# Kernel tuning notes

Measured on AMD Instinct MI355X. Metric: run time of the kernel, lower is better.

## Reference

```python
import jax, jax.numpy as jnp
import numpy as np
import math

B, T, C = 2, 512, 1024
E, TOPK = 8, 2
NH, HS = 8, 128  # att_hidden = NH*HS = 1024
AH = NH * HS


def setup_inputs() -> dict:
    key = jax.random.key(0)
    ks = jax.random.split(key, 8)
    s = 0.02
    return {
        "x": jax.random.normal(ks[0], (B, T, C), dtype=jnp.float32),
        "Wg": jax.random.normal(ks[1], (C, E), dtype=jnp.float32) * s,
        "W_in": jax.random.normal(ks[2], (E, C, AH), dtype=jnp.float32) * s,
        "W_out": jax.random.normal(ks[3], (E, AH, C), dtype=jnp.float32) * s,
        "Wk": jax.random.normal(ks[4], (C, AH), dtype=jnp.float32) * s,
        "bk": jnp.zeros((AH,), dtype=jnp.float32),
        "Wv": jax.random.normal(ks[5], (C, AH), dtype=jnp.float32) * s,
        "bv": jnp.zeros((AH,), dtype=jnp.float32),
    }


def stickbreaking(logits, mask, cum_weight):
    # logits: [B, i, j, k, h]; mask/cum_weight: [i, j] (tril / strict tril)
    log_z = jax.nn.log_sigmoid(logits)
    m = mask[None, :, :, None, None]
    log_beta = jnp.where(m == 0, 0.0, log_z - logits)  # log(1-sigmoid)
    # cumulative sum of log_beta over earlier positions: [b,i,j,n,h] x [j,k] -> [b,i,k,n,h]
    re_cum_log_beta = jnp.einsum('bijnh,jk->biknh', log_beta, cum_weight)
    return jnp.where(m == 0, 0.0, jnp.exp(log_z + re_cum_log_beta))


def reference(x, Wg, W_in, W_out, Wk, bk, Wv, bv):
    Bx, Tx, Cx = x.shape
    # --- MoE q_proj.map: top-k expert routing ---
    gate_logits = jnp.einsum('btc,ce->bte', x, Wg)
    top_vals, top_idx = jax.lax.top_k(gate_logits, TOPK)        # [B,T,K]
    gates = jax.nn.softmax(top_vals, axis=-1)                    # [B,T,K]
    all_q = jnp.einsum('btc,ech->bteh', x, W_in)                 # [B,T,E,AH]
    q = jnp.take_along_axis(all_q, top_idx[..., None], axis=2)   # [B,T,K,AH]
    # aux load-balancing loss (switch-style)
    probs = jax.nn.softmax(gate_logits, axis=-1)                 # [B,T,E]
    disp = jax.nn.one_hot(top_idx, E, dtype=x.dtype)             # [B,T,K,E]
    frac = disp.sum(axis=2).reshape(-1, E).mean(axis=0)
    aux_loss = E * jnp.sum(probs.reshape(-1, E).mean(axis=0) * frac)

    k = x @ Wk + bk
    v = x @ Wv + bv

    q = q.reshape(Bx, Tx, TOPK, NH, HS)
    k = k.reshape(Bx, Tx, NH, HS)
    v = v.reshape(Bx, Tx, NH, HS)

    tril = jnp.tril(jnp.ones((Tx, Tx), dtype=x.dtype))
    mask = tril                                   # history_length=0 -> ctx==T
    cum_weight = jnp.tril(tril, -1)

    att = jnp.einsum('bikhd,bjhd->bijkh', q, k) * (1.0 / math.sqrt(HS))
    att = stickbreaking(att, mask, cum_weight)    # [B,T,T,K,NH]

    y = jnp.einsum('bijkh,bjhd->bikhd', att, v)   # [B,T,K,NH,HS]
    y = y.reshape(Bx, Tx, TOPK, AH)

    # --- MoE q_proj.reduce: per-expert output proj, gate-weighted combine ---
    yw = y * gates[..., None]                     # [B,T,K,AH]
    comb = jnp.einsum('btkh,btke->bteh', yw, disp)  # [B,T,E,AH]
    out = jnp.einsum('bteh,ehc->btc', comb, W_out)  # [B,T,C]
    return out, aux_loss
```

## Files before the change

### kernel.cpp

```cpp
#include <hip/hip_runtime.h>
#include <cmath>

#define B_    2
#define T_    512
#define C_    1024
#define E_    8
#define NTOK  1024
#define NPAIR 2048
#define AH_   1024
#define NH_   8
#define HS_   128

typedef unsigned short u16;
typedef __attribute__((ext_vector_type(8))) short bf16x8;
typedef __attribute__((ext_vector_type(4))) float f32x4;

__device__ __forceinline__ u16 f2bf(float f) {
    union { float f; unsigned u; } v; v.f = f;
    unsigned r = v.u + 0x7fff + ((v.u >> 16) & 1);
    return (u16)(r >> 16);
}

typedef const __attribute__((address_space(1))) unsigned int ga_u32;
typedef __attribute__((address_space(3))) unsigned int ls_u32;
__device__ __forceinline__ void gld_lds16(const u16* g, u16* l) {
    __builtin_amdgcn_global_load_lds((ga_u32*)g, (ls_u32*)l, 16, 0, 0);
}

__device__ __forceinline__ void atomic_fadd(float* p, float v) {
    __hip_atomic_fetch_add(p, v, __ATOMIC_RELAXED, __HIP_MEMORY_SCOPE_AGENT);
}

__global__ __launch_bounds__(64) void gate_kernel(
    const float* __restrict__ x, const float* __restrict__ Wg,
    u16* __restrict__ xb, float* __restrict__ gates,
    float* __restrict__ probs, int* __restrict__ eass,
    float* __restrict__ out)
{
    int token = blockIdx.x;
    int lane  = threadIdx.x;
    {
        float4 z4 = {0.f, 0.f, 0.f, 0.f};
        float4* orow = (float4*)(out + (size_t)token * C_);
#pragma unroll
        for (int i = 0; i < 4; i++) orow[lane + i * 64] = z4;
    }
    const float* xr = x + (size_t)token * C_;
    u16* xbr = xb + (size_t)token * C_;
    float acc[E_];
#pragma unroll
    for (int e = 0; e < E_; e++) acc[e] = 0.f;
    for (int c = lane; c < C_; c += 64) {
        float xv = xr[c];
        xbr[c] = f2bf(xv);
        const float* wr = Wg + c * E_;
#pragma unroll
        for (int e = 0; e < E_; e++) acc[e] += xv * wr[e];
    }
#pragma unroll
    for (int e = 0; e < E_; e++) {
        float v = acc[e];
        v += __shfl_xor(v, 32); v += __shfl_xor(v, 16); v += __shfl_xor(v, 8);
        v += __shfl_xor(v, 4);  v += __shfl_xor(v, 2);  v += __shfl_xor(v, 1);
        acc[e] = v;
    }
    if (lane == 0) {
        int i0 = 0; float v0 = acc[0];
        for (int e = 1; e < E_; e++) if (acc[e] > v0) { v0 = acc[e]; i0 = e; }
        int i1 = -1; float v1 = -3.4e38f;
        for (int e = 0; e < E_; e++) if (e != i0 && acc[e] > v1) { v1 = acc[e]; i1 = e; }
        float e1  = __expf(v1 - v0);
        float inv = 1.f / (1.f + e1);
        gates[token * 2 + 0] = inv;
        gates[token * 2 + 1] = e1 * inv;
        float s = 0.f; float pe[E_];
        for (int e = 0; e < E_; e++) { pe[e] = __expf(acc[e] - v0); s += pe[e]; }
        float sinv = 1.f / s;
        for (int e = 0; e < E_; e++) probs[token * E_ + e] = pe[e] * sinv;
        eass[token * 2 + 0] = i0;
        eass[token * 2 + 1] = i1;
    }
}

__global__ __launch_bounds__(256) void route_kernel(
    const float* __restrict__ probs, const int* __restrict__ eass,
    const float* __restrict__ bk, const float* __restrict__ bv,
    int* __restrict__ bucket_cnt, int* __restrict__ buckets,
    float* __restrict__ bkv, float* __restrict__ aux_out)
{
    __shared__ float red[256][17];
    __shared__ int lcnt[E_];
    int tid = threadIdx.x;
    for (int i = tid; i < 1024; i += 256) {
        bkv[i] = bk[i];
        bkv[i + 1024] = bv[i];
    }
    float ps[E_], fc[E_];
#pragma unroll
    for (int e = 0; e < E_; e++) { ps[e] = 0.f; fc[e] = 0.f; }
    for (int k = 0; k < 4; k++) {
        int row = tid + k * 256;
#pragma unroll
        for (int e = 0; e < E_; e++) ps[e] += probs[row * E_ + e];
    }
    for (int k = 0; k < 8; k++) {
        int i = tid + k * 256;
        int ea = eass[i];
#pragma unroll
        for (int e = 0; e < E_; e++) fc[e] += (ea == e) ? 1.f : 0.f;
    }
#pragma unroll
    for (int e = 0; e < E_; e++) { red[tid][e] = ps[e]; red[tid][8 + e] = fc[e]; }
    if (tid < E_) lcnt[tid] = 0;
    __syncthreads();
    for (int s = 128; s > 0; s >>= 1) {
        if (tid < s)
#pragma unroll
            for (int j = 0; j < 16; j++) red[tid][j] += red[tid + s][j];
        __syncthreads();
    }
    if (tid == 0) {
        float s = 0.f;
        for (int e = 0; e < E_; e++)
            s += (red[0][e] * (1.f / 1024.f)) * (red[0][8 + e] * (1.f / 1024.f));
        aux_out[0] = (float)E_ * s;
    }
    for (int k = 0; k < 8; k++) {
        int i = tid + k * 256;
        int ea = eass[i];
        int pos = atomicAdd(&lcnt[ea], 1);
        buckets[ea * NPAIR + pos] = i;
    }
    __syncthreads();
    if (tid < E_) bucket_cnt[tid] = lcnt[tid];
}

__global__ __launch_bounds__(256) void pack_all(
    const float* __restrict__ Win, const float* __restrict__ Wout,
    const float* __restrict__ Wk, const float* __restrict__ Wv,
    u16* __restrict__ wp, u16* __restrict__ woutp, u16* __restrict__ wkvp)
{
    __shared__ float t[64][65];
    int z = blockIdx.z;
    const float* src; u16* dst;
    if (z < 8)       { src = Win  + ((size_t)z << 20);       dst = wp    + ((size_t)z << 20); }
    else if (z < 16) { src = Wout + ((size_t)(z - 8) << 20); dst = woutp + ((size_t)(z - 8) << 20); }
    else if (z == 16){ src = Wk;                             dst = wkvp; }
    else             { src = Wv;                             dst = wkvp + ((size_t)1 << 20); }
    int k0 = blockIdx.y * 64, n0 = blockIdx.x * 64;
    int tid = threadIdx.x;
#pragma unroll
    for (int p = 0; p < 4; p++) {
        int e4 = tid + 256 * p;
        int r = e4 >> 4, c4 = e4 & 15;
        float4 v = *(const float4*)&src[(size_t)(k0 + r) * 1024 + n0 + c4 * 4];
        t[r][c4 * 4 + 0] = v.x; t[r][c4 * 4 + 1] = v.y;
        t[r][c4 * 4 + 2] = v.z; t[r][c4 * 4 + 3] = v.w;
    }
    __syncthreads();
    int c = tid & 63, ks_rel = (tid >> 6) & 1, ph = tid >> 7;
    int n_glob = n0 + c, nt = n_glob >> 7, n_loc = n_glob & 127;
    int ks = (k0 >> 5) + ks_rel;
    u16* ob = dst + (((size_t)(nt * 32 + ks)) << 12) + n_loc * 32;
#pragma unroll
    for (int pp = 0; pp < 2; pp++) {
        int p = ph * 2 + pp;
        int g = (p - ((n_loc >> 1) & 3)) & 3;
        int kb = ks_rel * 32 + g * 8;
        ushort4 o1, o2;
        o1.x = f2bf(t[kb + 0][c]); o1.y = f2bf(t[kb + 1][c]);
        o1.z = f2bf(t[kb + 2][c]); o1.w = f2bf(t[kb + 3][c]);
        o2.x = f2bf(t[kb + 4][c]); o2.y = f2bf(t[kb + 5][c]);
        o2.z = f2bf(t[kb + 6][c]); o2.w = f2bf(t[kb + 7][c]);
        *(ushort4*)&ob[p * 8]     = o1;
        *(ushort4*)&ob[p * 8 + 4] = o2;
    }
}

__device__ __forceinline__ void mfma_lds_loop(
    const u16* __restrict__ Aptr,
    const u16* __restrict__ Bsrc,
    u16* __restrict__ ldsB,
    int tid, f32x4 acc[8])
{
    int w = tid >> 6, lane = tid & 63, lm = lane & 15, g = lane >> 4;
    int swz = (g + ((lm >> 1) & 3)) & 3;
    const u16* gstage = Bsrc + w * 512 + lane * 8;
    u16* lstage = ldsB + w * 512;
    const u16* bbase = ldsB + lm * 32 + swz * 8;

#pragma unroll
    for (int c = 0; c < 4; c++)
        gld_lds16(gstage + c * 2048, lstage + c * 2048);

    bf16x8 a0 = *(const bf16x8*)(Aptr);
    bf16x8 a1 = *(const bf16x8*)(Aptr + 32);
    __syncthreads();

#pragma unroll
    for (int kk = 0; kk < 16; kk++) {
        int cur = kk & 1;
        if (kk < 15) {
            const u16* gs = gstage + (size_t)(kk + 1) * 8192;
            u16* ls = lstage + ((kk + 1) & 1) * 8192;
#pragma unroll
            for (int c = 0; c < 4; c++)
                gld_lds16(gs + c * 2048, ls + c * 2048);
        }
        bf16x8 na0, na1;
        if (kk < 15) {
            na0 = *(const bf16x8*)(Aptr + (size_t)(2 * kk + 2) * 32);
            na1 = *(const bf16x8*)(Aptr + (size_t)(2 * kk + 3) * 32);
        }
        const u16* bb = bbase + cur * 8192;
#pragma unroll
        for (int j = 0; j < 8; j++) {
            bf16x8 b0 = *(const bf16x8*)(bb + j * 512);
            acc[j] = __builtin_amdgcn_mfma_f32_16x16x32_bf16(a0, b0, acc[j], 0, 0, 0);
        }
#pragma unroll
        for (int j = 0; j < 8; j++) {
            bf16x8 b1 = *(const bf16x8*)(bb + 4096 + j * 512);
            acc[j] = __builtin_amdgcn_mfma_f32_16x16x32_bf16(a1, b1, acc[j], 0, 0, 0);
        }
        a0 = na0; a1 = na1;
        __syncthreads();
    }
}

__global__ __launch_bounds__(256) void gemm_fused(
    const u16* __restrict__ xb, const u16* __restrict__ Wkv_p,
    const float* __restrict__ bkv, const u16* __restrict__ Win_p,
    const int* __restrict__ bucket_cnt, const int* __restrict__ buckets,
    u16* __restrict__ Kb, u16* __restrict__ Vb, u16* __restrict__ Qb)
{
    __shared__ __align__(16) u16 ldsB[2 * 8192];
    int bx = blockIdx.x;
    int tid = threadIdx.x;
    int w = tid >> 6, lane = tid & 63, lm = lane & 15, g = lane >> 4;
    bool isKV = bx < 256;
    int e = 0, mt, nt, cnt;
    const u16* Wp;
    if (isKV) {
        mt = bx & 15; nt = bx >> 4; cnt = NTOK; Wp = Wkv_p;
    } else {
        int b2 = bx - 256;
        mt = b2 >> 6; e = (b2 & 63) >> 3; nt = b2 & 7;
        cnt = bucket_cnt[e];
        Wp = Win_p + ((size_t)e << 20);
    }
    int m0 = mt * 64;
    if (m0 >= cnt) return;
    int strip = m0 + w * 16;

    int arow, drow[4];
    if (isKV) {
        arow = strip + lm;
#pragma unroll
        for (int r = 0; r < 4; r++) drow[r] = strip + g * 4 + r;
    } else {
        int ai = strip + lm;
        arow = buckets[e * NPAIR + (ai < cnt ? ai : cnt - 1)] >> 1;
#pragma unroll
        for (int r = 0; r < 4; r++) {
            int di = strip + g * 4 + r;
            drow[r] = (di < cnt) ? buckets[e * NPAIR + di] : -1;
        }
    }
    const u16* Aptr = xb + (size_t)arow * 1024 + g * 8;
    const u16* Bsrc = Wp + (((size_t)(nt * 32)) << 12);

    f32x4 acc[8];
#pragma unroll
    for (int j = 0; j < 8; j++) acc[j] = 0;

    mfma_lds_loop(Aptr, Bsrc, ldsB, tid, acc);

#pragma unroll
    for (int reg = 0; reg < 4; reg++) {
        int di = strip + g * 4 + reg;
        if (isKV || di < cnt) {
            int orow = drow[reg];
            if (!isKV && orow < 0) continue;
#pragma unroll
            for (int j = 0; j < 8; j++) {
                int col = nt * 128 + j * 16 + lm;
                float v = acc[j][reg];
                if (isKV) {
                    v += bkv[col];
                    int tb = orow >> 9, tj = orow & 511;
                    int cc = col & 1023;
                    int hh = cc >> 7, dd = cc & 127;
                    u16* dst = (col < 1024) ? Kb : Vb;
                    dst[(((size_t)(tb * 8 + hh) * 512 + tj) << 7) + dd] = f2bf(v);
                } else {
                    int pb = orow >> 10, pi = (orow >> 1) & 511, ps = orow & 1;
                    int hh = col >> 7, dd = col & 127;
                    Qb[((((size_t)(pb * 16 + ps * 8 + hh)) * 512 + pi) << 7) + dd] = f2bf(v);
                }
            }
        }
    }
}

__global__ __launch_bounds__(256) void gemm_wout(
    const u16* __restrict__ yb, const u16* __restrict__ Wout_p,
    const int* __restrict__ bucket_cnt, const int* __restrict__ buckets,
    float* __restrict__ Out)
{
    __shared__ __align__(16) u16 ldsB[2 * 8192];
    int bx = blockIdx.x;
    int tid = threadIdx.x;
    int w = tid >> 6, lane = tid & 63, lm = lane & 15, g = lane >> 4;
    int mt = bx >> 6, e = (bx & 63) >> 3, nt = bx & 7;
    int cnt = bucket_cnt[e];
    int m0 = mt * 64;
    if (m0 >= cnt) return;
    int strip = m0 + w * 16;

    int ai = strip + lm;
    int arow = buckets[e * NPAIR + (ai < cnt ? ai : cnt - 1)];
    int drow[4];
#pragma unroll
    for (int r = 0; r < 4; r++) {
        int di = strip + g * 4 + r;
        drow[r] = (di < cnt) ? buckets[e * NPAIR + di] : -1;
    }
    const u16* Aptr = yb + (size_t)arow * 1024 + g * 8;
    const u16* Bsrc = Wout_p + ((size_t)e << 20) + (((size_t)(nt * 32)) << 12);

    f32x4 acc[8];
#pragma unroll
    for (int j = 0; j < 8; j++) acc[j] = 0;

    mfma_lds_loop(Aptr, Bsrc, ldsB, tid, acc);

#pragma unroll
    for (int reg = 0; reg < 4; reg++) {
        int orow = drow[reg];
        if (orow >= 0) {
            float* od = Out + (size_t)(orow >> 1) * 1024;
#pragma unroll
            for (int j = 0; j < 8; j++) {
                int col = nt * 128 + j * 16 + lm;
                atomic_fadd(&od[col], acc[j][reg]);
            }
        }
    }
}

__global__ __launch_bounds__(256) void vtrans(
    const u16* __restrict__ Vb, u16* __restrict__ Vtb)
{
    __shared__ u16 t[64][72];
    int bh = blockIdx.x;
    int d0 = blockIdx.y * 64;
    int j0 = blockIdx.z * 64;
    int tid = threadIdx.x;
#pragma unroll
    for (int p = 0; p < 2; p++) {
        int c = tid + 256 * p;
        int jr = c >> 3, c8 = c & 7;
        *(bf16x8*)&t[jr][c8 * 8] =
            *(const bf16x8*)&Vb[((size_t)bh * 512 + j0 + jr) * 128 + d0 + c8 * 8];
    }
    __syncthreads();
#pragma unroll
    for (int p = 0; p < 2; p++) {
        int c = tid + 256 * p;
        int dr = c >> 3, j8 = c & 7;
        bf16x8 o;
#pragma unroll
        for (int k = 0; k < 8; k++) o[k] = (short)t[j8 * 8 + k][dr];
        *(bf16x8*)&Vtb[((size_t)bh * 128 + d0 + dr) * 512 + j0 + j8 * 8] = o;
    }
}

__global__ __launch_bounds__(256) void attn_kernel(
    const u16* __restrict__ Qb, const u16* __restrict__ Kb,
    const u16* __restrict__ Vtb, const float* __restrict__ gates,
    u16* __restrict__ yb)
{
    __shared__ __align__(16) u16 Qs[32 * 136];
    __shared__ __align__(16) u16 Ks[2][32 * 136];
    __shared__ __align__(16) u16 Vts[2][128 * 40];
    __shared__ __align__(16) float sw[32 * 36];
    __shared__ __align__(16) u16 wt[32 * 40];

    int combo = blockIdx.x;
    int b = combo >> 4, slot = (combo >> 3) & 1, h = combo & 7;
    int bh = b * 8 + h;
    const u16* Qbase = Qb  + ((size_t)combo << 16);
    const u16* Kbase = Kb  + ((size_t)bh << 16);
    const u16* Vbase = Vtb + ((size_t)bh << 16);

    int tid = threadIdx.x;
    int w = tid >> 6, lane = tid & 63, lm = lane & 15, g = lane >> 4;
    int mh = w >> 1, nh = w & 1, dsel = w & 1;
    int srow = tid >> 3, st = tid & 7;
    int rowlane = lane & 56;
    const float SCALE2 = 0.127517433f;

    int by = blockIdx.y;
    int it = (by < 8) ? (15 - by) : (by - 8);
    int i0 = it * 32;

    int kr0 = tid >> 4, kc = (tid & 15) * 8;
    int vr0 = tid >> 2, vc = (tid & 3) * 8;
    bf16x8 kreg[2], vreg[2];

#define LDKV(j0_)                                                                  \
    {                                                                              \
        _Pragma("unroll")                                                          \
        for (int p = 0; p < 2; p++) {                                              \
            kreg[p] = *(const bf16x8*)&Kbase[(size_t)((j0_) + kr0 + 16 * p) * 128 + kc]; \
            vreg[p] = *(const bf16x8*)&Vbase[(size_t)(vr0 + 64 * p) * 512 + (j0_) + vc]; \
        }                                                                          \
    }
#define STKV(buf_)                                                                 \
    {                                                                              \
        _Pragma("unroll")                                                          \
        for (int p = 0; p < 2; p++) {                                              \
            *(bf16x8*)&Ks[buf_][(kr0 + 16 * p) * 136 + kc] = kreg[p];              \
            *(bf16x8*)&Vts[buf_][(vr0 + 64 * p) * 40 + vc] = vreg[p];              \
        }                                                                          \
    }

#pragma unroll
    for (int p = 0; p < 2; p++) {
        int c = tid + 256 * p;
        int r = c >> 4, c8 = c & 15;
        *(bf16x8*)&Qs[r * 136 + c8 * 8] =
            *(const bf16x8*)&Qbase[(size_t)(i0 + r) * 128 + c8 * 8];
    }
    LDKV(i0);
    STKV(0);
    __syncthreads();

    f32x4 pacc[4];
#pragma unroll
    for (int q = 0; q < 4; q++) pacc[q] = 0;
    float running = 0.f;
    int pbuf = 0;

    for (int jt = it; jt >= 0; jt--) {
        int j0 = jt * 32;
        f32x4 sacc = 0;
#pragma unroll
        for (int ks = 0; ks < 4; ks++) {
            bf16x8 aq = *(const bf16x8*)&Qs[(mh * 16 + lm) * 136 + ks * 32 + g * 8];
            bf16x8 bk = *(const bf16x8*)&Ks[pbuf][(nh * 16 + lm) * 136 + ks * 32 + g * 8];
            sacc = __builtin_amdgcn_mfma_f32_16x16x32_bf16(aq, bk, sacc, 0, 0, 0);
        }
#pragma unroll
        for (int reg = 0; reg < 4; reg++)
            sw[(mh * 16 + g * 4 + reg) * 36 + nh * 16 + lm] = sacc[reg] * SCALE2;
        if (jt > 0) LDKV(j0 - 32);
        __syncthreads();
        {
            float4 sv = *(const float4*)&sw[srow * 36 + st * 4];
            float sarr[4] = {sv.x, sv.y, sv.z, sv.w};
            int ig = i0 + srow;
            float lsig[4], lb[4];
#pragma unroll
            for (int c2 = 0; c2 < 4; c2++) {
                int jg = j0 + st * 4 + c2;
                float sc = sarr[c2];
                float a  = fabsf(sc);
                float tl = __builtin_amdgcn_logf(1.f + __builtin_amdgcn_exp2f(-a));
                lsig[c2] = (sc >= 0.f) ? -tl : sc - tl;
                lb[c2]   = (jg <= ig) ? -(tl + fmaxf(sc, 0.f)) : 0.f;
            }
            float suf[4];
            suf[3] = 0.f;
            suf[2] = lb[3];
            suf[1] = lb[2] + lb[3];
            suf[0] = lb[1] + suf[1];
            float total = lb[0] + suf[0];
            float incl = total;
            float y1 = __shfl_down(incl, 1, 64); if (st < 7) incl += y1;
            float y2 = __shfl_down(incl, 2, 64); if (st < 6) incl += y2;
            float y4 = __shfl_down(incl, 4, 64); if (st < 4) incl += y4;
            float basev = (incl - total) + running;
            ushort4 wo;
            float wv;
            int jgc = j0 + st * 4;
            wv = (jgc + 0 <= ig) ? __builtin_amdgcn_exp2f(lsig[0] + suf[0] + basev) : 0.f; wo.x = f2bf(wv);
            wv = (jgc + 1 <= ig) ? __builtin_amdgcn_exp2f(lsig[1] + suf[1] + basev) : 0.f; wo.y = f2bf(wv);
            wv = (jgc + 2 <= ig) ? __builtin_amdgcn_exp2f(lsig[2] + suf[2] + basev) : 0.f; wo.z = f2bf(wv);
            wv = (jgc + 3 <= ig) ? __builtin_amdgcn_exp2f(lsig[3] + suf[3] + basev) : 0.f; wo.w = f2bf(wv);
            running += __shfl(incl, rowlane, 64);
            *(ushort4*)&wt[srow * 40 + st * 4] = wo;
        }
        if (jt > 0) STKV(pbuf ^ 1);
        __syncthreads();
        bf16x8 aw = *(const bf16x8*)&wt[(mh * 16 + lm) * 40 + g * 8];
#pragma unroll
        for (int q = 0; q < 4; q++) {
            int dt = q * 2 + dsel;
            bf16x8 bv8 = *(const bf16x8*)&Vts[pbuf][(dt * 16 + lm) * 40 + g * 8];
            pacc[q] = __builtin_amdgcn_mfma_f32_16x16x32_bf16(aw, bv8, pacc[q], 0, 0, 0);
        }
        pbuf ^= 1;
    }
#pragma unroll
    for (int reg = 0; reg < 4; reg++) {
        int i = i0 + mh * 16 + g * 4 + reg;
        size_t pair = ((size_t)(b * 512 + i)) * 2 + slot;
        float gt = gates[pair];
#pragma unroll
        for (int q = 0; q < 4; q++) {
            int d = (q * 2 + dsel) * 16 + lm;
            yb[pair * 1024 + h * 128 + d] = f2bf(pacc[q][reg] * gt);
        }
    }
#undef LDKV
#undef STKV
}

extern "C" void kernel_launch(void* const* d_in, const int* in_sizes, int n_in,
                              void* d_out, int out_size, void* d_ws, size_t ws_size,
                              hipStream_t stream)
{
    const float* x     = (const float*)d_in[0];
    const float* Wg    = (const float*)d_in[1];
    const float* W_in  = (const float*)d_in[2];
    const float* W_out = (const float*)d_in[3];
    const float* Wk    = (const float*)d_in[4];
    const float* bk    = (const float*)d_in[5];
    const float* Wv    = (const float*)d_in[6];
    const float* bv    = (const float*)d_in[7];

    char* ws = (char*)d_ws;
    int*   bucket_cnt = (int*)ws;
    size_t off = 256;
    float* gates = (float*)(ws + off); off += (size_t)NPAIR * 4;
    int* buckets = (int*)(ws + off);   off += (size_t)E_ * NPAIR * 4;
    float* bkv   = (float*)(ws + off); off += 2048 * 4;
    float* probs = (float*)(ws + off); off += (size_t)NTOK * E_ * 4;
    int*   eass  = (int*)(ws + off);   off += (size_t)NPAIR * 4;
    off = (off + 255) & ~(size_t)255;
    u16* xb     = (u16*)(ws + off); off += (size_t)NTOK * C_ * 2;
    u16* Wkv_p  = (u16*)(ws + off); off += (size_t)2048 * 1024 * 2;
    u16* wp     = (u16*)(ws + off); off += (size_t)E_ * 1024 * 1024 * 2;
    u16* wout_p = (u16*)(ws + off); off += (size_t)E_ * 1024 * 1024 * 2;
    u16* yb     = (u16*)(ws + off); off += (size_t)NPAIR * AH_ * 2;
    u16* Qbuf   = (u16*)(ws + off); off += (size_t)32 * 512 * 128 * 2;
    u16* Kbuf   = (u16*)(ws + off); off += (size_t)16 * 512 * 128 * 2;
    u16* Vbuf   = (u16*)(ws + off); off += (size_t)16 * 512 * 128 * 2;
    u16* Vtbuf  = (u16*)(ws + off); off += (size_t)16 * 128 * 512 * 2;

    gate_kernel<<<NTOK, 64, 0, stream>>>(x, Wg, xb, gates, probs, eass,
                                         (float*)d_out);
    route_kernel<<<1, 256, 0, stream>>>(probs, eass, bk, bv, bucket_cnt,
                                        buckets, bkv,
                                        (float*)d_out + (out_size - 1));
    pack_all<<<dim3(16, 16, 18), 256, 0, stream>>>(W_in, W_out, Wk, Wv,
                                                   wp, wout_p, Wkv_p);

    gemm_fused<<<256 + 2048, 256, 0, stream>>>(xb, Wkv_p, bkv, wp, bucket_cnt,
                                               buckets, Kbuf, Vbuf, Qbuf);
    vtrans<<<dim3(16, 2, 8), 256, 0, stream>>>(Vbuf, Vtbuf);

    attn_kernel<<<dim3(32, 16), 256, 0, stream>>>(Qbuf, Kbuf, Vtbuf, gates, yb);

    gemm_wout<<<2048, 256, 0, stream>>>(yb, wout_p, bucket_cnt, buckets,
                                        (float*)d_out);
}
```

Before: 206.6 us.

## Merge gate into weight-pack kernel and fuse V transpose into GEMM epilogue

The gating/x-to-bf16 kernel and the bias copy are folded into the weight packing kernel as extra blocks on a flattened 1D grid, so one launch replaces two. The V transpose kernel is removed: KV GEMM tiles for V columns are staged through LDS and written directly in transposed layout, avoiding a round trip through an intermediate V buffer. This reduces launch count and global traffic, but reuses the GEMM's LDS buffer after the MFMA loop and adds a branchy epilogue.

Result: faster. 198.5 us (-3.9%).

```diff
diff --git a/kernel.cpp b/kernel.cpp
--- a/kernel.cpp
+++ b/kernel.cpp
@@ -31,124 +31,82 @@
     __hip_atomic_fetch_add(p, v, __ATOMIC_RELAXED, __HIP_MEMORY_SCOPE_AGENT);
 }
 
-__global__ __launch_bounds__(64) void gate_kernel(
+__global__ __launch_bounds__(256) void pack_gate(
+    const float* __restrict__ Win, const float* __restrict__ Wout,
+    const float* __restrict__ Wk, const float* __restrict__ Wv,
+    u16* __restrict__ wp, u16* __restrict__ woutp, u16* __restrict__ wkvp,
     const float* __restrict__ x, const float* __restrict__ Wg,
     u16* __restrict__ xb, float* __restrict__ gates,
     float* __restrict__ probs, int* __restrict__ eass,
-    float* __restrict__ out)
-{
-    int token = blockIdx.x;
-    int lane  = threadIdx.x;
-    {
-        float4 z4 = {0.f, 0.f, 0.f, 0.f};
-        float4* orow = (float4*)(out + (size_t)token * C_);
-#pragma unroll
-        for (int i = 0; i < 4; i++) orow[lane + i * 64] = z4;
-    }
-    const float* xr = x + (size_t)token * C_;
-    u16* xbr = xb + (size_t)token * C_;
-    float acc[E_];
-#pragma unroll
-    for (int e = 0; e < E_; e++) acc[e] = 0.f;
-    for (int c = lane; c < C_; c += 64) {
-        float xv = xr[c];
-        xbr[c] = f2bf(xv);
-        const float* wr = Wg + c * E_;
-#pragma unroll
-        for (int e = 0; e < E_; e++) acc[e] += xv * wr[e];
-    }
-#pragma unroll
-    for (int e = 0; e < E_; e++) {
-        float v = acc[e];
-        v += __shfl_xor(v, 32); v += __shfl_xor(v, 16); v += __shfl_xor(v, 8);
-        v += __shfl_xor(v, 4);  v += __shfl_xor(v, 2);  v += __shfl_xor(v, 1);
-        acc[e] = v;
-    }
-    if (lane == 0) {
-        int i0 = 0; float v0 = acc[0];
-        for (int e = 1; e < E_; e++) if (acc[e] > v0) { v0 = acc[e]; i0 = e; }
-        int i1 = -1; float v1 = -3.4e38f;
-        for (int e = 0; e < E_; e++) if (e != i0 && acc[e] > v1) { v1 = acc[e]; i1 = e; }
-        float e1  = __expf(v1 - v0);
-        float inv = 1.f / (1.f + e1);
-        gates[token * 2 + 0] = inv;
-        gates[token * 2 + 1] = e1 * inv;
-        float s = 0.f; float pe[E_];
-        for (int e = 0; e < E_; e++) { pe[e] = __expf(acc[e] - v0); s += pe[e]; }
-        float sinv = 1.f / s;
-        for (int e = 0; e < E_; e++) probs[token * E_ + e] = pe[e] * sinv;
-        eass[token * 2 + 0] = i0;
-        eass[token * 2 + 1] = i1;
-    }
-}
-
-__global__ __launch_bounds__(256) void route_kernel(
-    const float* __restrict__ probs, const int* __restrict__ eass,
+    float* __restrict__ out,
     const float* __restrict__ bk, const float* __restrict__ bv,
-    int* __restrict__ bucket_cnt, int* __restrict__ buckets,
-    float* __restrict__ bkv, float* __restrict__ aux_out)
-{
-    __shared__ float red[256][17];
-    __shared__ int lcnt[E_];
+    float* __restrict__ bkv)
+{
+    __shared__ float t[64][65];
+    int bx = blockIdx.x;
     int tid = threadIdx.x;
-    for (int i = tid; i < 1024; i += 256) {
-        bkv[i] = bk[i];
-        bkv[i + 1024] = bv[i];
-    }
-    float ps[E_], fc[E_];
-#pragma unroll
-    for (int e = 0; e < E_; e++) { ps[e] = 0.f; fc[e] = 0.f; }
-    for (int k = 0; k < 4; k++) {
-        int row = tid + k * 256;
-#pragma unroll
-        for (int e = 0; e < E_; e++) ps[e] += probs[row * E_ + e];
-    }
-    for (int k = 0; k < 8; k++) {
-        int i = tid + k * 256;
-        int ea = eass[i];
-#pragma unroll
-        for (int e = 0; e < E_; e++) fc[e] += (ea == e) ? 1.f : 0.f;
-    }
-#pragma unroll
-    for (int e = 0; e < E_; e++) { red[tid][e] = ps[e]; red[tid][8 + e] = fc[e]; }
-    if (tid < E_) lcnt[tid] = 0;
-    __syncthreads();
-    for (int s = 128; s > 0; s >>= 1) {
-        if (tid < s)
-#pragma unroll
-            for (int j = 0; j < 16; j++) red[tid][j] += red[tid + s][j];
-        __syncthreads();
-    }
-    if (tid == 0) {
-        float s = 0.f;
-        for (int e = 0; e < E_; e++)
-            s += (red[0][e] * (1.f / 1024.f)) * (red[0][8 + e] * (1.f / 1024.f));
-        aux_out[0] = (float)E_ * s;
-    }
-    for (int k = 0; k < 8; k++) {
-        int i = tid + k * 256;
-        int ea = eass[i];
-        int pos = atomicAdd(&lcnt[ea], 1);
-        buckets[ea * NPAIR + pos] = i;
-    }
-    __syncthreads();
-    if (tid < E_) bucket_cnt[tid] = lcnt[tid];
-}
-
-__global__ __launch_bounds__(256) void pack_all(
-    const float* __restrict__ Win, const float* __restrict__ Wout,
-    const float* __restrict__ Wk, const float* __restrict__ Wv,
-    u16* __restrict__ wp, u16* __restrict__ woutp, u16* __restrict__ wkvp)
-{
-    __shared__ float t[64][65];
-    int z = blockIdx.z;
+
+    if (bx >= 4608) {
+        if (bx == 4864) {
+            for (int i = tid; i < 1024; i += 256) {
+                bkv[i] = bk[i];
+                bkv[i + 1024] = bv[i];
+            }
+            return;
+        }
+        int w = tid >> 6, lane = tid & 63;
+        int token = (bx - 4608) * 4 + w;
+        {
+            float4 z4 = {0.f, 0.f, 0.f, 0.f};
+            float4* orow = (float4*)(out + (size_t)token * C_);
+#pragma unroll
+            for (int i = 0; i < 4; i++) orow[lane + i * 64] = z4;
+        }
+        const float* xr = x + (size_t)token * C_;
+        u16* xbr = xb + (size_t)token * C_;
+        float acc[E_];
+#pragma unroll
+        for (int e = 0; e < E_; e++) acc[e] = 0.f;
+        for (int c = lane; c < C_; c += 64) {
+            float xv = xr[c];
+            xbr[c] = f2bf(xv);
+            const float* wr = Wg + c * E_;
+#pragma unroll
+            for (int e = 0; e < E_; e++) acc[e] += xv * wr[e];
+        }
+#pragma unroll
+        for (int e = 0; e < E_; e++) {
+            float v = acc[e];
+            v += __shfl_xor(v, 32); v += __shfl_xor(v, 16); v += __shfl_xor(v, 8);
+            v += __shfl_xor(v, 4);  v += __shfl_xor(v, 2);  v += __shfl_xor(v, 1);
+            acc[e] = v;
+        }
+        if (lane == 0) {
+            int i0 = 0; float v0 = acc[0];
+            for (int e = 1; e < E_; e++) if (acc[e] > v0) { v0 = acc[e]; i0 = e; }
+            int i1 = -1; float v1 = -3.4e38f;
+            for (int e = 0; e < E_; e++) if (e != i0 && acc[e] > v1) { v1 = acc[e]; i1 = e; }
+            float e1  = __expf(v1 - v0);
+            float inv = 1.f / (1.f + e1);
+            gates[token * 2 + 0] = inv;
+            gates[token * 2 + 1] = e1 * inv;
+            float s = 0.f; float pe[E_];
+            for (int e = 0; e < E_; e++) { pe[e] = __expf(acc[e] - v0); s += pe[e]; }
+            float sinv = 1.f / s;
+            for (int e = 0; e < E_; e++) probs[token * E_ + e] = pe[e] * sinv;
+            eass[token * 2 + 0] = i0;
+            eass[token * 2 + 1] = i1;
+        }
+        return;
+    }
+
+    int z = bx >> 8, yy = (bx >> 4) & 15, xx = bx & 15;
     const float* src; u16* dst;
-    if (z < 8)       { src = Win  + ((size_t)z << 20);       dst = wp    + ((size_t)z << 20); }
-    else if (z < 16) { src = Wout + ((size_t)(z - 8) << 20); dst = woutp + ((size_t)(z - 8) << 20); }
-    else if (z == 16){ src = Wk;                             dst = wkvp; }
-    else             { src = Wv;                             dst = wkvp + ((size_t)1 << 20); }
-    int k0 = blockIdx.y * 64, n0 = blockIdx.x * 64;
-    int tid = threadIdx.x;
+    if (z < 8)        { src = Win  + ((size_t)z << 20);       dst = wp    + ((size_t)z << 20); }
+    else if (z < 16)  { src = Wout + ((size_t)(z - 8) << 20); dst = woutp + ((size_t)(z - 8) << 20); }
+    else if (z == 16) { src = Wk;                             dst = wkvp; }
+    else              { src = Wv;                             dst = wkvp + ((size_t)1 << 20); }
+    int k0 = yy * 64, n0 = xx * 64;
 #pragma unroll
     for (int p = 0; p < 4; p++) {
         int e4 = tid + 256 * p;
@@ -177,6 +135,54 @@
     }
 }
 
+__global__ __launch_bounds__(256) void route_kernel(
+    const float* __restrict__ probs, const int* __restrict__ eass,
+    int* __restrict__ bucket_cnt, int* __restrict__ buckets,
+    float* __restrict__ aux_out)
+{
+    __shared__ float red[256][17];
+    __shared__ int lcnt[E_];
+    int tid = threadIdx.x;
+    float ps[E_], fc[E_];
+#pragma unroll
+    for (int e = 0; e < E_; e++) { ps[e] = 0.f; fc[e] = 0.f; }
+    for (int k = 0; k < 4; k++) {
+        int row = tid + k * 256;
+#pragma unroll
+        for (int e = 0; e < E_; e++) ps[e] += probs[row * E_ + e];
+    }
+    for (int k = 0; k < 8; k++) {
+        int i = tid + k * 256;
+        int ea = eass[i];
+#pragma unroll
+        for (int e = 0; e < E_; e++) fc[e] += (ea == e) ? 1.f : 0.f;
+    }
+#pragma unroll
+    for (int e = 0; e < E_; e++) { red[tid][e] = ps[e]; red[tid][8 + e] = fc[e]; }
+    if (tid < E_) lcnt[tid] = 0;
+    __syncthreads();
+    for (int s = 128; s > 0; s >>= 1) {
+        if (tid < s)
+#pragma unroll
+            for (int j = 0; j < 16; j++) red[tid][j] += red[tid + s][j];
+        __syncthreads();
+    }
+    if (tid == 0) {
+        float s = 0.f;
+        for (int e = 0; e < E_; e++)
+            s += (red[0][e] * (1.f / 1024.f)) * (red[0][8 + e] * (1.f / 1024.f));
+        aux_out[0] = (float)E_ * s;
+    }
+    for (int k = 0; k < 8; k++) {
+        int i = tid + k * 256;
+        int ea = eass[i];
+        int pos = atomicAdd(&lcnt[ea], 1);
+        buckets[ea * NPAIR + pos] = i;
+    }
+    __syncthreads();
+    if (tid < E_) bucket_cnt[tid] = lcnt[tid];
+}
+
 __device__ __forceinline__ void mfma_lds_loop(
     const u16* __restrict__ Aptr,
     const u16* __restrict__ Bsrc,
@@ -232,7 +238,7 @@
     const u16* __restrict__ xb, const u16* __restrict__ Wkv_p,
     const float* __restrict__ bkv, const u16* __restrict__ Win_p,
     const int* __restrict__ bucket_cnt, const int* __restrict__ buckets,
-    u16* __restrict__ Kb, u16* __restrict__ Vb, u16* __restrict__ Qb)
+    u16* __restrict__ Kb, u16* __restrict__ Vtb, u16* __restrict__ Qb)
 {
     __shared__ __align__(16) u16 ldsB[2 * 8192];
     int bx = blockIdx.x;
@@ -276,6 +282,33 @@
 
     mfma_lds_loop(Aptr, Bsrc, ldsB, tid, acc);
 
+    if (isKV && nt >= 8) {
+        u16* tt = ldsB;
+#pragma unroll
+        for (int reg = 0; reg < 4; reg++) {
+            int r_loc = w * 16 + g * 4 + reg;
+#pragma unroll
+            for (int j = 0; j < 8; j++) {
+                int col = nt * 128 + j * 16 + lm;
+                tt[r_loc * 136 + j * 16 + lm] = f2bf(acc[j][reg] + bkv[col]);
+            }
+        }
+        __syncthreads();
+        int hh = nt - 8;
+        int tb = m0 >> 9, tj0 = m0 & 511;
+        int bh = tb * 8 + hh;
+#pragma unroll
+        for (int p = 0; p < 4; p++) {
+            int cc = tid + 256 * p;
+            int dr = cc >> 3, j8 = cc & 7;
+            bf16x8 o;
+#pragma unroll
+            for (int k = 0; k < 8; k++) o[k] = (short)tt[(j8 * 8 + k) * 136 + dr];
+            *(bf16x8*)&Vtb[((size_t)bh * 128 + dr) * 512 + tj0 + j8 * 8] = o;
+        }
+        return;
+    }
+
 #pragma unroll
     for (int reg = 0; reg < 4; reg++) {
         int di = strip + g * 4 + reg;
@@ -289,10 +322,8 @@
                 if (isKV) {
                     v += bkv[col];
                     int tb = orow >> 9, tj = orow & 511;
-                    int cc = col & 1023;
-                    int hh = cc >> 7, dd = cc & 127;
-                    u16* dst = (col < 1024) ? Kb : Vb;
-                    dst[(((size_t)(tb * 8 + hh) * 512 + tj) << 7) + dd] = f2bf(v);
+                    int hh = col >> 7, dd = col & 127;
+                    Kb[(((size_t)(tb * 8 + hh) * 512 + tj) << 7) + dd] = f2bf(v);
                 } else {
                     int pb = orow >> 10, pi = (orow >> 1) & 511, ps = orow & 1;
                     int hh = col >> 7, dd = col & 127;
@@ -346,33 +377,6 @@
                 atomic_fadd(&od[col], acc[j][reg]);
             }
         }
-    }
-}
-
-__global__ __launch_bounds__(256) void vtrans(
-    const u16* __restrict__ Vb, u16* __restrict__ Vtb)
-{
-    __shared__ u16 t[64][72];
-    int bh = blockIdx.x;
-    int d0 = blockIdx.y * 64;
-    int j0 = blockIdx.z * 64;
-    int tid = threadIdx.x;
-#pragma unroll
-    for (int p = 0; p < 2; p++) {
-        int c = tid + 256 * p;
-        int jr = c >> 3, c8 = c & 7;
-        *(bf16x8*)&t[jr][c8 * 8] =
-            *(const bf16x8*)&Vb[((size_t)bh * 512 + j0 + jr) * 128 + d0 + c8 * 8];
-    }
-    __syncthreads();
-#pragma unroll
-    for (int p = 0; p < 2; p++) {
-        int c = tid + 256 * p;
-        int dr = c >> 3, j8 = c & 7;
-        bf16x8 o;
-#pragma unroll
-        for (int k = 0; k < 8; k++) o[k] = (short)t[j8 * 8 + k][dr];
-        *(bf16x8*)&Vtb[((size_t)bh * 128 + d0 + dr) * 512 + j0 + j8 * 8] = o;
     }
 }
 
@@ -547,20 +551,16 @@
     u16* yb     = (u16*)(ws + off); off += (size_t)NPAIR * AH_ * 2;
     u16* Qbuf   = (u16*)(ws + off); off += (size_t)32 * 512 * 128 * 2;
     u16* Kbuf   = (u16*)(ws + off); off += (size_t)16 * 512 * 128 * 2;
-    u16* Vbuf   = (u16*)(ws + off); off += (size_t)16 * 512 * 128 * 2;
     u16* Vtbuf  = (u16*)(ws + off); off += (size_t)16 * 128 * 512 * 2;
 
-    gate_kernel<<<NTOK, 64, 0, stream>>>(x, Wg, xb, gates, probs, eass,
-                                         (float*)d_out);
-    route_kernel<<<1, 256, 0, stream>>>(probs, eass, bk, bv, bucket_cnt,
-                                        buckets, bkv,
+    pack_gate<<<4865, 256, 0, stream>>>(W_in, W_out, Wk, Wv, wp, wout_p, Wkv_p,
+                                        x, Wg, xb, gates, probs, eass,
+                                        (float*)d_out, bk, bv, bkv);
+    route_kernel<<<1, 256, 0, stream>>>(probs, eass, bucket_cnt, buckets,
                                         (float*)d_out + (out_size - 1));
-    pack_all<<<dim3(16, 16, 18), 256, 0, stream>>>(W_in, W_out, Wk, Wv,
-                                                   wp, wout_p, Wkv_p);
 
     gemm_fused<<<256 + 2048, 256, 0, stream>>>(xb, Wkv_p, bkv, wp, bucket_cnt,
-                                               buckets, Kbuf, Vbuf, Qbuf);
-    vtrans<<<dim3(16, 2, 8), 256, 0, stream>>>(Vbuf, Vtbuf);
+                                               buckets, Kbuf, Vtbuf, Qbuf);
 
     attn_kernel<<<dim3(32, 16), 256, 0, stream>>>(Qbuf, Kbuf, Vtbuf, gates, yb);
 
```
